# Performance work log

Hardware: AMD Instinct MI355X
Metric: run time of the kernel (lower is better)

The kernel has to match this reference:

```python
import jax, jax.numpy as jnp
import numpy as np

NUM_EXPERTS = 64
TOP_K = 2
AUX_COEF = 0.001
Z_COEF = 0.001


def setup_inputs() -> dict:
    key = jax.random.key(0)
    k1, k2 = jax.random.split(key)
    hidden_states = jax.random.normal(k1, (16384, 4096), dtype=jnp.float32)
    W_gate = jax.random.normal(k2, (NUM_EXPERTS, 4096), dtype=jnp.float32) * 0.02
    return {"hidden_states": hidden_states, "W_gate": W_gate}


def reference(hidden_states, W_gate):
    # Gate GEMM: [N, H] x [E, H]^T -> [N, E]
    router_logits = jnp.einsum('nh,eh->ne', hidden_states, W_gate)
    router_probs = jax.nn.softmax(router_logits, axis=-1)

    # Top-k selection + renormalization
    expert_weights, expert_indices = jax.lax.top_k(router_probs, TOP_K)
    expert_weights = expert_weights / jnp.sum(expert_weights, axis=-1, keepdims=True)

    # Load-balancing loss: num_experts * sum_i f_i * P_i
    num_tokens = router_probs.shape[0]
    one_hot = jax.nn.one_hot(expert_indices, NUM_EXPERTS, dtype=jnp.float32)  # [N, K, E]
    tokens_per_expert = one_hot.sum(axis=(0, 1))  # [E]
    f = tokens_per_expert / (num_tokens * TOP_K)
    P = router_probs.mean(axis=0)
    lb_loss = NUM_EXPERTS * jnp.sum(f * P)

    # Z-loss: mean of logsumexp(logits)^2
    log_z = jax.nn.logsumexp(router_logits, axis=-1)
    z_loss = jnp.mean(log_z ** 2)

    aux_loss = AUX_COEF * lb_loss + Z_COEF * z_loss
    return expert_weights, expert_indices, aux_loss
```

## Files before the change

### kernel.cpp

```cpp
#include <hip/hip_runtime.h>
#include <hip/hip_bf16.h>

#define NTOK 16384
#define HD   4096
#define NE   64
#define TTILE 32
#define NBLK (NTOK / TTILE)
#define NIT  (HD / 32)

#define SAB 40
#define SL  68

#define WS_ACC_FLOATS 192
#define B_ELEMS (NE * HD)

typedef __bf16 bf16x8 __attribute__((ext_vector_type(8)));
typedef __bf16 bf16x4 __attribute__((ext_vector_type(4)));
typedef float  f32x4  __attribute__((ext_vector_type(4)));

__device__ __forceinline__ f32x4 mfma16(bf16x8 a, bf16x8 b, f32x4 c) {
    return __builtin_amdgcn_mfma_f32_16x16x32_bf16(a, b, c, 0, 0, 0);
}

__device__ __forceinline__ void cvt_split(float4 v, bf16x4& hi, bf16x4& lo) {
    float x[4] = {v.x, v.y, v.z, v.w};
    #pragma unroll
    for (int e = 0; e < 4; ++e) {
        __bf16 h = (__bf16)x[e];
        hi[e] = h;
        lo[e] = (__bf16)(x[e] - (float)h);
    }
}

__global__ void zero_ws_kernel(float* ws) {
    int i = threadIdx.x;
    if (i < 129) ws[i] = 0.0f;
}

__global__ __launch_bounds__(256) void prep_kernel(
    const float* __restrict__ Wg, float* __restrict__ ws)
{
    const int tid = threadIdx.x;
    if (blockIdx.x == 0 && tid < 129) ws[tid] = 0.0f;
    __bf16* Bhi = (__bf16*)(ws + WS_ACC_FLOATS);
    __bf16* Blo = Bhi + B_ELEMS;
    const int i = (blockIdx.x * 256 + tid) * 8;
    float4 v0 = *(const float4*)(Wg + i);
    float4 v1 = *(const float4*)(Wg + i + 4);
    bf16x4 h0, l0, h1, l1;
    cvt_split(v0, h0, l0);
    cvt_split(v1, h1, l1);
    *(bf16x4*)(Bhi + i)     = h0;
    *(bf16x4*)(Bhi + i + 4) = h1;
    *(bf16x4*)(Blo + i)     = l0;
    *(bf16x4*)(Blo + i + 4) = l1;
}

__global__ __launch_bounds__(256) void router_pre_kernel(
    const float* __restrict__ hs,
    const __bf16* __restrict__ Bhi,
    const __bf16* __restrict__ Blo,
    float* __restrict__ out,
    float* __restrict__ ws)
{
    __shared__ __bf16 sAhi[2][TTILE * SAB];
    __shared__ __bf16 sAlo[2][TTILE * SAB];
    __shared__ float  sLog[TTILE * SL];
    __shared__ float  sInv[TTILE];
    __shared__ float  sPp[4 * 64];
    __shared__ float  sCnt[64];
    __shared__ float  sZ;

    const int tid = threadIdx.x;
    const int t0  = blockIdx.x * TTILE;

    if (tid < 64) sCnt[tid] = 0.0f;
    if (tid == 0) sZ = 0.0f;

    const int r1 = tid >> 3;
    const int c4 = (tid & 7) * 4;
    const float* gA = hs + (size_t)(t0 + r1) * HD + c4;
    const int oA = r1 * SAB + c4;

    const int lane = tid & 63;
    const int wv   = tid >> 6;
    const int wr   = (wv >> 1) * 16;
    const int wc   = (wv & 1) * 32;
    const int fm   = lane & 15;
    const int fq   = lane >> 4;
    const int fk   = fq * 8;

    const __bf16* gBh = Bhi + (size_t)(wc + fm) * HD + fk;
    const __bf16* gBl = Blo + (size_t)(wc + fm) * HD + fk;

    f32x4 acc[2];
    acc[0] = (f32x4){0.f, 0.f, 0.f, 0.f};
    acc[1] = (f32x4){0.f, 0.f, 0.f, 0.f};

    {
        float4 a0 = *(const float4*)(gA);
        bf16x4 h, l;
        cvt_split(a0, h, l);
        *(bf16x4*)&sAhi[0][oA] = h;
        *(bf16x4*)&sAlo[0][oA] = l;
    }
    bf16x8 cbh[2], cbl[2];
    cbh[0] = *(const bf16x8*)(gBh);
    cbh[1] = *(const bf16x8*)(gBh + 16 * HD);
    cbl[0] = *(const bf16x8*)(gBl);
    cbl[1] = *(const bf16x8*)(gBl + 16 * HD);
    __syncthreads();

    #pragma unroll 2
    for (int it = 0; it < NIT; ++it) {
        const int cur = it & 1;
        const bool more = (it + 1) < NIT;

        float4 na;
        bf16x8 nbh0, nbh1, nbl0, nbl1;
        if (more) {
            const int k0 = (it + 1) * 32;
            na   = *(const float4*)(gA + k0);
            nbh0 = *(const bf16x8*)(gBh + k0);
            nbh1 = *(const bf16x8*)(gBh + 16 * HD + k0);
            nbl0 = *(const bf16x8*)(gBl + k0);
            nbl1 = *(const bf16x8*)(gBl + 16 * HD + k0);
        }

        bf16x8 ahi, alo;
        {
            const int aoff = (wr + fm) * SAB + fk;
            ahi = *(const bf16x8*)&sAhi[cur][aoff];
            alo = *(const bf16x8*)&sAlo[cur][aoff];
        }
        acc[0] = mfma16(ahi, cbh[0], acc[0]);
        acc[0] = mfma16(ahi, cbl[0], acc[0]);
        acc[0] = mfma16(alo, cbh[0], acc[0]);
        acc[0] = mfma16(alo, cbl[0], acc[0]);
        acc[1] = mfma16(ahi, cbh[1], acc[1]);
        acc[1] = mfma16(ahi, cbl[1], acc[1]);
        acc[1] = mfma16(alo, cbh[1], acc[1]);
        acc[1] = mfma16(alo, cbl[1], acc[1]);

        if (more) {
            bf16x4 h, l;
            cvt_split(na, h, l);
            *(bf16x4*)&sAhi[cur ^ 1][oA] = h;
            *(bf16x4*)&sAlo[cur ^ 1][oA] = l;
            cbh[0] = nbh0; cbh[1] = nbh1;
            cbl[0] = nbl0; cbl[1] = nbl1;
        }
        __syncthreads();
    }

    #pragma unroll
    for (int j = 0; j < 2; ++j)
        #pragma unroll
        for (int r = 0; r < 4; ++r) {
            const int tokl = wr + fq * 4 + r;
            const int expl = wc + j * 16 + fm;
            sLog[tokl * SL + expl] = acc[j][r];
        }
    __syncthreads();

    const int g = tid >> 3;
    const int l = tid & 7;
    float* Lrow = &sLog[g * SL + l * 8];
    float lv[8];
    float m = -3.0e38f;
    #pragma unroll
    for (int c = 0; c < 8; ++c) { lv[c] = Lrow[c]; m = fmaxf(m, lv[c]); }
    m = fmaxf(m, __shfl_xor(m, 1, 64));
    m = fmaxf(m, __shfl_xor(m, 2, 64));
    m = fmaxf(m, __shfl_xor(m, 4, 64));

    float v1 = -3.0e38f, v2 = -3.0e38f; int i1 = 0, i2 = 0;
    float ssum = 0.0f;
    #pragma unroll
    for (int c = 0; c < 8; ++c) {
        const float val = lv[c]; const int idx = l * 8 + c;
        const float ev = __expf(val - m);
        Lrow[c] = ev;
        ssum += ev;
        if (val > v1) { v2 = v1; i2 = i1; v1 = val; i1 = idx; }
        else if (val > v2) { v2 = val; i2 = idx; }
    }
    ssum += __shfl_xor(ssum, 1, 64);
    ssum += __shfl_xor(ssum, 2, 64);
    ssum += __shfl_xor(ssum, 4, 64);

    #pragma unroll
    for (int s = 1; s <= 4; s <<= 1) {
        const float ov1 = __shfl_xor(v1, s, 64);
        const int   oi1 = __shfl_xor(i1, s, 64);
        const float ov2 = __shfl_xor(v2, s, 64);
        const int   oi2 = __shfl_xor(i2, s, 64);
        float n1, n2; int ni1, ni2;
        const bool ofirst = (ov1 > v1) || (ov1 == v1 && oi1 < i1);
        if (ofirst) {
            n1 = ov1; ni1 = oi1;
            const bool osec = (ov2 > v1) || (ov2 == v1 && oi2 < i1);
            n2 = osec ? ov2 : v1; ni2 = osec ? oi2 : i1;
        } else {
            n1 = v1; ni1 = i1;
            const bool asec = (v2 > ov1) || (v2 == ov1 && i2 < oi1);
            n2 = asec ? v2 : ov1; ni2 = asec ? i2 : oi1;
        }
        v1 = n1; i1 = ni1; v2 = n2; i2 = ni2;
    }

    if (l == 0) {
        const float e1 = __expf(v1 - m), e2 = __expf(v2 - m);
        const float winv = 1.0f / (e1 + e2);
        const int token = t0 + g;
        out[2 * token]     = e1 * winv;
        out[2 * token + 1] = e2 * winv;
        out[2 * NTOK + 2 * token]     = (float)i1;
        out[2 * NTOK + 2 * token + 1] = (float)i2;
        const float lse = m + __logf(ssum);
        atomicAdd(&sZ, lse * lse);
        atomicAdd(&sCnt[i1], 1.0f);
        atomicAdd(&sCnt[i2], 1.0f);
        sInv[g] = 1.0f / ssum;
    }
    __syncthreads();

    {
        const int e = tid & 63;
        const int q = tid >> 6;
        float part = 0.0f;
        #pragma unroll
        for (int t = 0; t < 8; ++t) {
            const int tok = q * 8 + t;
            part += sLog[tok * SL + e] * sInv[tok];
        }
        sPp[q * 64 + e] = part;
    }
    __syncthreads();
    if (tid < 64) {
        const float ps = sPp[tid] + sPp[64 + tid] + sPp[128 + tid] + sPp[192 + tid];
        atomicAdd(&ws[tid], ps);
        atomicAdd(&ws[64 + tid], sCnt[tid]);
    }
    if (tid == 0) atomicAdd(&ws[128], sZ);
}

__global__ __launch_bounds__(256) void router_fb_kernel(
    const float* __restrict__ hs,
    const float* __restrict__ Wg,
    float* __restrict__ out,
    float* __restrict__ ws)
{
    __shared__ __bf16 sAhi[2][TTILE * SAB];
    __shared__ __bf16 sAlo[2][TTILE * SAB];
    __shared__ __bf16 sBhi[2][NE * SAB];
    __shared__ __bf16 sBlo[2][NE * SAB];
    __shared__ float  sLog[TTILE * SL];
    __shared__ float  sInv[TTILE];
    __shared__ float  sPp[4 * 64];
    __shared__ float  sCnt[64];
    __shared__ float  sZ;

    const int tid = threadIdx.x;
    const int t0  = blockIdx.x * TTILE;

    if (tid < 64) sCnt[tid] = 0.0f;
    if (tid == 0) sZ = 0.0f;

    const int r1 = tid >> 3;
    const int c4 = (tid & 7) * 4;
    const float* gA = hs + (size_t)(t0 + r1) * HD + c4;
    const float* gB = Wg + (size_t)r1 * HD + c4;
    const int oA  = r1 * SAB + c4;
    const int oB1 = r1 * SAB + c4;
    const int oB2 = (r1 + 32) * SAB + c4;

    const int lane = tid & 63;
    const int wv   = tid >> 6;
    const int wr   = (wv >> 1) * 16;
    const int wc   = (wv & 1) * 32;
    const int fm   = lane & 15;
    const int fq   = lane >> 4;
    const int fk   = fq * 8;

    f32x4 acc[2];
    acc[0] = (f32x4){0.f, 0.f, 0.f, 0.f};
    acc[1] = (f32x4){0.f, 0.f, 0.f, 0.f};

    {
        float4 a0 = *(const float4*)(gA);
        float4 b0 = *(const float4*)(gB);
        float4 b1 = *(const float4*)(gB + 32 * HD);
        bf16x4 h, l;
        cvt_split(a0, h, l); *(bf16x4*)&sAhi[0][oA]  = h; *(bf16x4*)&sAlo[0][oA]  = l;
        cvt_split(b0, h, l); *(bf16x4*)&sBhi[0][oB1] = h; *(bf16x4*)&sBlo[0][oB1] = l;
        cvt_split(b1, h, l); *(bf16x4*)&sBhi[0][oB2] = h; *(bf16x4*)&sBlo[0][oB2] = l;
    }
    __syncthreads();

    for (int it = 0; it < NIT; ++it) {
        const int cur = it & 1;
        const bool more = (it + 1) < NIT;
        float4 na0, nb0, nb1;
        if (more) {
            const int k0 = (it + 1) * 32;
            na0 = *(const float4*)(gA + k0);
            nb0 = *(const float4*)(gB + k0);
            nb1 = *(const float4*)(gB + 32 * HD + k0);
        }

        bf16x8 ahi, alo, bhi[2], blo[2];
        {
            const int aoff = (wr + fm) * SAB + fk;
            ahi = *(const bf16x8*)&sAhi[cur][aoff];
            alo = *(const bf16x8*)&sAlo[cur][aoff];
        }
        #pragma unroll
        for (int j = 0; j < 2; ++j) {
            const int boff = (wc + j * 16 + fm) * SAB + fk;
            bhi[j] = *(const bf16x8*)&sBhi[cur][boff];
            blo[j] = *(const bf16x8*)&sBlo[cur][boff];
        }
        #pragma unroll
        for (int j = 0; j < 2; ++j) {
            acc[j] = mfma16(ahi, bhi[j], acc[j]);
            acc[j] = mfma16(ahi, blo[j], acc[j]);
            acc[j] = mfma16(alo, bhi[j], acc[j]);
            acc[j] = mfma16(alo, blo[j], acc[j]);
        }

        if (more) {
            const int nb = cur ^ 1;
            bf16x4 h, l;
            cvt_split(na0, h, l); *(bf16x4*)&sAhi[nb][oA]  = h; *(bf16x4*)&sAlo[nb][oA]  = l;
            cvt_split(nb0, h, l); *(bf16x4*)&sBhi[nb][oB1] = h; *(bf16x4*)&sBlo[nb][oB1] = l;
            cvt_split(nb1, h, l); *(bf16x4*)&sBhi[nb][oB2] = h; *(bf16x4*)&sBlo[nb][oB2] = l;
        }
        __syncthreads();
    }

    #pragma unroll
    for (int j = 0; j < 2; ++j)
        #pragma unroll
        for (int r = 0; r < 4; ++r) {
            const int tokl = wr + fq * 4 + r;
            const int expl = wc + j * 16 + fm;
            sLog[tokl * SL + expl] = acc[j][r];
        }
    __syncthreads();

    const int g = tid >> 3;
    const int l = tid & 7;
    float* Lrow = &sLog[g * SL + l * 8];
    float lv[8];
    float m = -3.0e38f;
    #pragma unroll
    for (int c = 0; c < 8; ++c) { lv[c] = Lrow[c]; m = fmaxf(m, lv[c]); }
    m = fmaxf(m, __shfl_xor(m, 1, 64));
    m = fmaxf(m, __shfl_xor(m, 2, 64));
    m = fmaxf(m, __shfl_xor(m, 4, 64));

    float v1 = -3.0e38f, v2 = -3.0e38f; int i1 = 0, i2 = 0;
    float ssum = 0.0f;
    #pragma unroll
    for (int c = 0; c < 8; ++c) {
        const float val = lv[c]; const int idx = l * 8 + c;
        const float ev = __expf(val - m);
        Lrow[c] = ev;
        ssum += ev;
        if (val > v1) { v2 = v1; i2 = i1; v1 = val; i1 = idx; }
        else if (val > v2) { v2 = val; i2 = idx; }
    }
    ssum += __shfl_xor(ssum, 1, 64);
    ssum += __shfl_xor(ssum, 2, 64);
    ssum += __shfl_xor(ssum, 4, 64);

    #pragma unroll
    for (int s = 1; s <= 4; s <<= 1) {
        const float ov1 = __shfl_xor(v1, s, 64);
        const int   oi1 = __shfl_xor(i1, s, 64);
        const float ov2 = __shfl_xor(v2, s, 64);
        const int   oi2 = __shfl_xor(i2, s, 64);
        float n1, n2; int ni1, ni2;
        const bool ofirst = (ov1 > v1) || (ov1 == v1 && oi1 < i1);
        if (ofirst) {
            n1 = ov1; ni1 = oi1;
            const bool osec = (ov2 > v1) || (ov2 == v1 && oi2 < i1);
            n2 = osec ? ov2 : v1; ni2 = osec ? oi2 : i1;
        } else {
            n1 = v1; ni1 = i1;
            const bool asec = (v2 > ov1) || (v2 == ov1 && i2 < oi1);
            n2 = asec ? v2 : ov1; ni2 = asec ? i2 : oi1;
        }
        v1 = n1; i1 = ni1; v2 = n2; i2 = ni2;
    }

    if (l == 0) {
        const float e1 = __expf(v1 - m), e2 = __expf(v2 - m);
        const float winv = 1.0f / (e1 + e2);
        const int token = t0 + g;
        out[2 * token]     = e1 * winv;
        out[2 * token + 1] = e2 * winv;
        out[2 * NTOK + 2 * token]     = (float)i1;
        out[2 * NTOK + 2 * token + 1] = (float)i2;
        const float lse = m + __logf(ssum);
        atomicAdd(&sZ, lse * lse);
        atomicAdd(&sCnt[i1], 1.0f);
        atomicAdd(&sCnt[i2], 1.0f);
        sInv[g] = 1.0f / ssum;
    }
    __syncthreads();

    {
        const int e = tid & 63;
        const int q = tid >> 6;
        float part = 0.0f;
        #pragma unroll
        for (int t = 0; t < 8; ++t) {
            const int tok = q * 8 + t;
            part += sLog[tok * SL + e] * sInv[tok];
        }
        sPp[q * 64 + e] = part;
    }
    __syncthreads();
    if (tid < 64) {
        const float ps = sPp[tid] + sPp[64 + tid] + sPp[128 + tid] + sPp[192 + tid];
        atomicAdd(&ws[tid], ps);
        atomicAdd(&ws[64 + tid], sCnt[tid]);
    }
    if (tid == 0) atomicAdd(&ws[128], sZ);
}

__global__ void finalize_kernel(const float* __restrict__ ws, float* __restrict__ out) {
    const int e = threadIdx.x;
    const float P = ws[e] * (1.0f / NTOK);
    const float f = ws[64 + e] * (1.0f / (NTOK * 2));
    float term = f * P;
    #pragma unroll
    for (int s = 32; s >= 1; s >>= 1) term += __shfl_xor(term, s, 64);
    if (e == 0) {
        const float lb = 64.0f * term;
        const float z  = ws[128] * (1.0f / NTOK);
        out[4 * NTOK] = 0.001f * lb + 0.001f * z;
    }
}

extern "C" void kernel_launch(void* const* d_in, const int* in_sizes, int n_in,
                              void* d_out, int out_size, void* d_ws, size_t ws_size,
                              hipStream_t stream) {
    const float* hs = (const float*)d_in[0];
    const float* Wg = (const float*)d_in[1];
    float* out = (float*)d_out;
    float* ws  = (float*)d_ws;

    const size_t need = (size_t)WS_ACC_FLOATS * sizeof(float)
                      + (size_t)B_ELEMS * 2 * sizeof(__bf16);
    if (ws_size >= need) {
        const __bf16* Bhi = (const __bf16*)(ws + WS_ACC_FLOATS);
        const __bf16* Blo = Bhi + B_ELEMS;
        hipLaunchKernelGGL(prep_kernel, dim3(128), dim3(256), 0, stream, Wg, ws);
        hipLaunchKernelGGL(router_pre_kernel, dim3(NBLK), dim3(256), 0, stream,
                           hs, Bhi, Blo, out, ws);
    } else {
        hipLaunchKernelGGL(zero_ws_kernel, dim3(1), dim3(256), 0, stream, ws);
        hipLaunchKernelGGL(router_fb_kernel, dim3(NBLK), dim3(256), 0, stream,
                           hs, Wg, out, ws);
    }
    hipLaunchKernelGGL(finalize_kernel, dim3(1), dim3(64), 0, stream, ws, out);
}
```

Baseline: 437.1 us.

## Rewrite pre-split router GEMM as register-pipelined 16-token tiles without LDS staging

The main router kernel now processes 16 tokens per block, with each of four waves owning 16 experts. Each lane loads its A fragment straight from global memory into registers and converts it to hi/lo bf16 in place, so the shared-memory staging and per-iteration __syncthreads are gone. A four-deep register prefetch ring keeps loads in flight, and launch bounds request higher occupancy. The cost is more register pressure, doubled B-fragment traffic per token (fewer tokens share each B load), and twice as many blocks doing atomics into the workspace.

```diff
diff --git a/kernel.cpp b/kernel.cpp
--- a/kernel.cpp
+++ b/kernel.cpp
@@ -4,9 +4,14 @@
 #define NTOK 16384
 #define HD   4096
 #define NE   64
-#define TTILE 32
-#define NBLK (NTOK / TTILE)
-#define NIT  (HD / 32)
+
+#define TPRE     16
+#define NBLK_PRE (NTOK / TPRE)
+#define KSTEPS   (HD / 32)
+
+#define TFB      32
+#define NBLK_FB  (NTOK / TFB)
+#define NIT      (HD / 32)
 
 #define SAB 40
 #define SL  68
@@ -30,6 +35,16 @@
         hi[e] = h;
         lo[e] = (__bf16)(x[e] - (float)h);
     }
+}
+
+__device__ __forceinline__ void cvt8(float4 x0, float4 x1, bf16x8& hi, bf16x8& lo) {
+    bf16x4 h, l;
+    cvt_split(x0, h, l);
+    #pragma unroll
+    for (int e = 0; e < 4; ++e) { hi[e] = h[e]; lo[e] = l[e]; }
+    cvt_split(x1, h, l);
+    #pragma unroll
+    for (int e = 0; e < 4; ++e) { hi[4 + e] = h[e]; lo[4 + e] = l[e]; }
 }
 
 __global__ void zero_ws_kernel(float* ws) {
@@ -56,23 +71,196 @@
     *(bf16x4*)(Blo + i + 4) = l1;
 }
 
-__global__ __launch_bounds__(256) void router_pre_kernel(
+__global__ __launch_bounds__(256, 4) void router_pre_kernel(
     const float* __restrict__ hs,
     const __bf16* __restrict__ Bhi,
     const __bf16* __restrict__ Blo,
     float* __restrict__ out,
     float* __restrict__ ws)
 {
-    __shared__ __bf16 sAhi[2][TTILE * SAB];
-    __shared__ __bf16 sAlo[2][TTILE * SAB];
-    __shared__ float  sLog[TTILE * SL];
-    __shared__ float  sInv[TTILE];
+    __shared__ float sLog[TPRE * SL];
+    __shared__ float sInv[TPRE];
+    __shared__ float sPp[4 * 64];
+    __shared__ float sCnt[64];
+    __shared__ float sZ;
+
+    const int tid = threadIdx.x;
+    const int t0  = blockIdx.x * TPRE;
+
+    if (tid < 64) sCnt[tid] = 0.0f;
+    if (tid == 0) sZ = 0.0f;
+
+    const int lane = tid & 63;
+    const int wv   = tid >> 6;
+    const int fm   = lane & 15;
+    const int fq   = lane >> 4;
+    const int fk   = fq * 8;
+
+    const float*  pA  = hs  + (size_t)(t0 + fm) * HD + fk;
+    const __bf16* pBh = Bhi + (size_t)(wv * 16 + fm) * HD + fk;
+    const __bf16* pBl = Blo + (size_t)(wv * 16 + fm) * HD + fk;
+
+    f32x4 acc = (f32x4){0.f, 0.f, 0.f, 0.f};
+
+    float4 fa0[4], fa1[4];
+    bf16x8 fbh[4], fbl[4];
+
+    #pragma unroll
+    for (int i = 0; i < 4; ++i) {
+        fa0[i] = *(const float4*)(pA + i * 32);
+        fa1[i] = *(const float4*)(pA + i * 32 + 4);
+        fbh[i] = *(const bf16x8*)(pBh + i * 32);
+        fbl[i] = *(const bf16x8*)(pBl + i * 32);
+    }
+
+#define STEP_LOAD(i, kb)                                                 \
+    {                                                                    \
+        bf16x8 ahi, alo;                                                 \
+        cvt8(fa0[i], fa1[i], ahi, alo);                                  \
+        acc = mfma16(ahi, fbh[i], acc);                                  \
+        acc = mfma16(ahi, fbl[i], acc);                                  \
+        acc = mfma16(alo, fbh[i], acc);                                  \
+        acc = mfma16(alo, fbl[i], acc);                                  \
+        const int nks = (kb) + (i) + 4;                                  \
+        fa0[i] = *(const float4*)(pA + nks * 32);                        \
+        fa1[i] = *(const float4*)(pA + nks * 32 + 4);                    \
+        fbh[i] = *(const bf16x8*)(pBh + nks * 32);                       \
+        fbl[i] = *(const bf16x8*)(pBl + nks * 32);                       \
+    }
+#define STEP_NOLOAD(i)                                                   \
+    {                                                                    \
+        bf16x8 ahi, alo;                                                 \
+        cvt8(fa0[i], fa1[i], ahi, alo);                                  \
+        acc = mfma16(ahi, fbh[i], acc);                                  \
+        acc = mfma16(ahi, fbl[i], acc);                                  \
+        acc = mfma16(alo, fbh[i], acc);                                  \
+        acc = mfma16(alo, fbl[i], acc);                                  \
+    }
+
+    for (int it = 0; it < (KSTEPS / 4) - 1; ++it) {
+        const int kb = it * 4;
+        STEP_LOAD(0, kb)
+        STEP_LOAD(1, kb)
+        STEP_LOAD(2, kb)
+        STEP_LOAD(3, kb)
+    }
+    STEP_NOLOAD(0)
+    STEP_NOLOAD(1)
+    STEP_NOLOAD(2)
+    STEP_NOLOAD(3)
+#undef STEP_LOAD
+#undef STEP_NOLOAD
+
+    #pragma unroll
+    for (int r = 0; r < 4; ++r) {
+        const int tokl = fq * 4 + r;
+        const int expl = wv * 16 + fm;
+        sLog[tokl * SL + expl] = acc[r];
+    }
+    __syncthreads();
+
+    const int g = tid >> 4;
+    const int l = tid & 15;
+    float* Lrow = &sLog[g * SL + l * 4];
+    float lv[4];
+    float m = -3.0e38f;
+    #pragma unroll
+    for (int c = 0; c < 4; ++c) { lv[c] = Lrow[c]; m = fmaxf(m, lv[c]); }
+    m = fmaxf(m, __shfl_xor(m, 1, 64));
+    m = fmaxf(m, __shfl_xor(m, 2, 64));
+    m = fmaxf(m, __shfl_xor(m, 4, 64));
+    m = fmaxf(m, __shfl_xor(m, 8, 64));
+
+    float v1 = -3.0e38f, v2 = -3.0e38f; int i1 = 0, i2 = 0;
+    float ssum = 0.0f;
+    #pragma unroll
+    for (int c = 0; c < 4; ++c) {
+        const float val = lv[c]; const int idx = l * 4 + c;
+        const float ev = __expf(val - m);
+        Lrow[c] = ev;
+        ssum += ev;
+        if (val > v1) { v2 = v1; i2 = i1; v1 = val; i1 = idx; }
+        else if (val > v2) { v2 = val; i2 = idx; }
+    }
+    ssum += __shfl_xor(ssum, 1, 64);
+    ssum += __shfl_xor(ssum, 2, 64);
+    ssum += __shfl_xor(ssum, 4, 64);
+    ssum += __shfl_xor(ssum, 8, 64);
+
+    #pragma unroll
+    for (int s = 1; s <= 8; s <<= 1) {
+        const float ov1 = __shfl_xor(v1, s, 64);
+        const int   oi1 = __shfl_xor(i1, s, 64);
+        const float ov2 = __shfl_xor(v2, s, 64);
+        const int   oi2 = __shfl_xor(i2, s, 64);
+        float n1, n2; int ni1, ni2;
+        const bool ofirst = (ov1 > v1) || (ov1 == v1 && oi1 < i1);
+        if (ofirst) {
+            n1 = ov1; ni1 = oi1;
+            const bool osec = (ov2 > v1) || (ov2 == v1 && oi2 < i1);
+            n2 = osec ? ov2 : v1; ni2 = osec ? oi2 : i1;
+        } else {
+            n1 = v1; ni1 = i1;
+            const bool asec = (v2 > ov1) || (v2 == ov1 && i2 < oi1);
+            n2 = asec ? v2 : ov1; ni2 = asec ? i2 : oi1;
+        }
+        v1 = n1; i1 = ni1; v2 = n2; i2 = ni2;
+    }
+
+    if (l == 0) {
+        const float e1 = __expf(v1 - m), e2 = __expf(v2 - m);
+        const float winv = 1.0f / (e1 + e2);
+        const int token = t0 + g;
+        out[2 * token]     = e1 * winv;
+        out[2 * token + 1] = e2 * winv;
+        out[2 * NTOK + 2 * token]     = (float)i1;
+        out[2 * NTOK + 2 * token + 1] = (float)i2;
+        const float lse = m + __logf(ssum);
+        atomicAdd(&sZ, lse * lse);
+        atomicAdd(&sCnt[i1], 1.0f);
+        atomicAdd(&sCnt[i2], 1.0f);
+        sInv[g] = 1.0f / ssum;
+    }
+    __syncthreads();
+
+    {
+        const int e = tid & 63;
+        const int q = tid >> 6;
+        float part = 0.0f;
+        #pragma unroll
+        for (int t = 0; t < 4; ++t) {
+            const int tok = q * 4 + t;
+            part += sLog[tok * SL + e] * sInv[tok];
+        }
+        sPp[q * 64 + e] = part;
+    }
+    __syncthreads();
+    if (tid < 64) {
+        const float ps = sPp[tid] + sPp[64 + tid] + sPp[128 + tid] + sPp[192 + tid];
+        atomicAdd(&ws[tid], ps);
+        atomicAdd(&ws[64 + tid], sCnt[tid]);
+    }
+    if (tid == 0) atomicAdd(&ws[128], sZ);
+}
+
+__global__ __launch_bounds__(256) void router_fb_kernel(
+    const float* __restrict__ hs,
+    const float* __restrict__ Wg,
+    float* __restrict__ out,
+    float* __restrict__ ws)
+{
+    __shared__ __bf16 sAhi[2][TFB * SAB];
+    __shared__ __bf16 sAlo[2][TFB * SAB];
+    __shared__ __bf16 sBhi[2][NE * SAB];
+    __shared__ __bf16 sBlo[2][NE * SAB];
+    __shared__ float  sLog[TFB * SL];
+    __shared__ float  sInv[TFB];
     __shared__ float  sPp[4 * 64];
     __shared__ float  sCnt[64];
     __shared__ float  sZ;
 
     const int tid = threadIdx.x;
-    const int t0  = blockIdx.x * TTILE;
+    const int t0  = blockIdx.x * TFB;
 
     if (tid < 64) sCnt[tid] = 0.0f;
     if (tid == 0) sZ = 0.0f;
@@ -80,7 +268,10 @@
     const int r1 = tid >> 3;
     const int c4 = (tid & 7) * 4;
     const float* gA = hs + (size_t)(t0 + r1) * HD + c4;
-    const int oA = r1 * SAB + c4;
+    const float* gB = Wg + (size_t)r1 * HD + c4;
+    const int oA  = r1 * SAB + c4;
+    const int oB1 = r1 * SAB + c4;
+    const int oB2 = (r1 + 32) * SAB + c4;
 
     const int lane = tid & 63;
     const int wv   = tid >> 6;
@@ -90,65 +281,58 @@
     const int fq   = lane >> 4;
     const int fk   = fq * 8;
 
-    const __bf16* gBh = Bhi + (size_t)(wc + fm) * HD + fk;
-    const __bf16* gBl = Blo + (size_t)(wc + fm) * HD + fk;
-
     f32x4 acc[2];
     acc[0] = (f32x4){0.f, 0.f, 0.f, 0.f};
     acc[1] = (f32x4){0.f, 0.f, 0.f, 0.f};
 
     {
         float4 a0 = *(const float4*)(gA);
+        float4 b0 = *(const float4*)(gB);
+        float4 b1 = *(const float4*)(gB + 32 * HD);
         bf16x4 h, l;
-        cvt_split(a0, h, l);
-        *(bf16x4*)&sAhi[0][oA] = h;
-        *(bf16x4*)&sAlo[0][oA] = l;
-    }
-    bf16x8 cbh[2], cbl[2];
-    cbh[0] = *(const bf16x8*)(gBh);
-    cbh[1] = *(const bf16x8*)(gBh + 16 * HD);
-    cbl[0] = *(const bf16x8*)(gBl);
-    cbl[1] = *(const bf16x8*)(gBl + 16 * HD);
-    __syncthreads();
-
-    #pragma unroll 2
+        cvt_split(a0, h, l); *(bf16x4*)&sAhi[0][oA]  = h; *(bf16x4*)&sAlo[0][oA]  = l;
+        cvt_split(b0, h, l); *(bf16x4*)&sBhi[0][oB1] = h; *(bf16x4*)&sBlo[0][oB1] = l;
+        cvt_split(b1, h, l); *(bf16x4*)&sBhi[0][oB2] = h; *(bf16x4*)&sBlo[0][oB2] = l;
+    }
+    __syncthreads();
+
     for (int it = 0; it < NIT; ++it) {
         const int cur = it & 1;
         const bool more = (it + 1) < NIT;
-
-        float4 na;
-        bf16x8 nbh0, nbh1, nbl0, nbl1;
+        float4 na0, nb0, nb1;
         if (more) {
             const int k0 = (it + 1) * 32;
-            na   = *(const float4*)(gA + k0);
-            nbh0 = *(const bf16x8*)(gBh + k0);
-            nbh1 = *(const bf16x8*)(gBh + 16 * HD + k0);
-            nbl0 = *(const bf16x8*)(gBl + k0);
-            nbl1 = *(const bf16x8*)(gBl + 16 * HD + k0);
-        }
-
-        bf16x8 ahi, alo;
+            na0 = *(const float4*)(gA + k0);
+            nb0 = *(const float4*)(gB + k0);
+            nb1 = *(const float4*)(gB + 32 * HD + k0);
+        }
+
+        bf16x8 ahi, alo, bhi[2], blo[2];
         {
             const int aoff = (wr + fm) * SAB + fk;
             ahi = *(const bf16x8*)&sAhi[cur][aoff];
             alo = *(const bf16x8*)&sAlo[cur][aoff];
         }
-        acc[0] = mfma16(ahi, cbh[0], acc[0]);
-        acc[0] = mfma16(ahi, cbl[0], acc[0]);
-        acc[0] = mfma16(alo, cbh[0], acc[0]);
-        acc[0] = mfma16(alo, cbl[0], acc[0]);
-        acc[1] = mfma16(ahi, cbh[1], acc[1]);
-        acc[1] = mfma16(ahi, cbl[1], acc[1]);
-        acc[1] = mfma16(alo, cbh[1], acc[1]);
-        acc[1] = mfma16(alo, cbl[1], acc[1]);
+        #pragma unroll
+        for (int j = 0; j < 2; ++j) {
+            const int boff = (wc + j * 16 + fm) * SAB + fk;
+            bhi[j] = *(const bf16x8*)&sBhi[cur][boff];
+            blo[j] = *(const bf16x8*)&sBlo[cur][boff];
+        }
+        #pragma unroll
+        for (int j = 0; j < 2; ++j) {
+            acc[j] = mfma16(ahi, bhi[j], acc[j]);
+            acc[j] = mfma16(ahi, blo[j], acc[j]);
+            acc[j] = mfma16(alo, bhi[j], acc[j]);
+            acc[j] = mfma16(alo, blo[j], acc[j]);
+        }
 
         if (more) {
+            const int nb = cur ^ 1;
             bf16x4 h, l;
-            cvt_split(na, h, l);
-            *(bf16x4*)&sAhi[cur ^ 1][oA] = h;
-            *(bf16x4*)&sAlo[cur ^ 1][oA] = l;
-            cbh[0] = nbh0; cbh[1] = nbh1;
-            cbl[0] = nbl0; cbl[1] = nbl1;
+            cvt_split(na0, h, l); *(bf16x4*)&sAhi[nb][oA]  = h; *(bf16x4*)&sAlo[nb][oA]  = l;
+            cvt_split(nb0, h, l); *(bf16x4*)&sBhi[nb][oB1] = h; *(bf16x4*)&sBlo[nb][oB1] = l;
+            cvt_split(nb1, h, l); *(bf16x4*)&sBhi[nb][oB2] = h; *(bf16x4*)&sBlo[nb][oB2] = l;
         }
         __syncthreads();
     }
@@ -245,192 +429,6 @@
     if (tid == 0) atomicAdd(&ws[128], sZ);
 }
 
-__global__ __launch_bounds__(256) void router_fb_kernel(
-    const float* __restrict__ hs,
-    const float* __restrict__ Wg,
-    float* __restrict__ out,
-    float* __restrict__ ws)
-{
-    __shared__ __bf16 sAhi[2][TTILE * SAB];
-    __shared__ __bf16 sAlo[2][TTILE * SAB];
-    __shared__ __bf16 sBhi[2][NE * SAB];
-    __shared__ __bf16 sBlo[2][NE * SAB];
-    __shared__ float  sLog[TTILE * SL];
-    __shared__ float  sInv[TTILE];
-    __shared__ float  sPp[4 * 64];
-    __shared__ float  sCnt[64];
-    __shared__ float  sZ;
-
-    const int tid = threadIdx.x;
-    const int t0  = blockIdx.x * TTILE;
-
-    if (tid < 64) sCnt[tid] = 0.0f;
-    if (tid == 0) sZ = 0.0f;
-
-    const int r1 = tid >> 3;
-    const int c4 = (tid & 7) * 4;
-    const float* gA = hs + (size_t)(t0 + r1) * HD + c4;
-    const float* gB = Wg + (size_t)r1 * HD + c4;
-    const int oA  = r1 * SAB + c4;
-    const int oB1 = r1 * SAB + c4;
-    const int oB2 = (r1 + 32) * SAB + c4;
-
-    const int lane = tid & 63;
-    const int wv   = tid >> 6;
-    const int wr   = (wv >> 1) * 16;
-    const int wc   = (wv & 1) * 32;
-    const int fm   = lane & 15;
-    const int fq   = lane >> 4;
-    const int fk   = fq * 8;
-
-    f32x4 acc[2];
-    acc[0] = (f32x4){0.f, 0.f, 0.f, 0.f};
-    acc[1] = (f32x4){0.f, 0.f, 0.f, 0.f};
-
-    {
-        float4 a0 = *(const float4*)(gA);
-        float4 b0 = *(const float4*)(gB);
-        float4 b1 = *(const float4*)(gB + 32 * HD);
-        bf16x4 h, l;
-        cvt_split(a0, h, l); *(bf16x4*)&sAhi[0][oA]  = h; *(bf16x4*)&sAlo[0][oA]  = l;
-        cvt_split(b0, h, l); *(bf16x4*)&sBhi[0][oB1] = h; *(bf16x4*)&sBlo[0][oB1] = l;
-        cvt_split(b1, h, l); *(bf16x4*)&sBhi[0][oB2] = h; *(bf16x4*)&sBlo[0][oB2] = l;
-    }
-    __syncthreads();
-
-    for (int it = 0; it < NIT; ++it) {
-        const int cur = it & 1;
-        const bool more = (it + 1) < NIT;
-        float4 na0, nb0, nb1;
-        if (more) {
-            const int k0 = (it + 1) * 32;
-            na0 = *(const float4*)(gA + k0);
-            nb0 = *(const float4*)(gB + k0);
-            nb1 = *(const float4*)(gB + 32 * HD + k0);
-        }
-
-        bf16x8 ahi, alo, bhi[2], blo[2];
-        {
-            const int aoff = (wr + fm) * SAB + fk;
-            ahi = *(const bf16x8*)&sAhi[cur][aoff];
-            alo = *(const bf16x8*)&sAlo[cur][aoff];
-        }
-        #pragma unroll
-        for (int j = 0; j < 2; ++j) {
-            const int boff = (wc + j * 16 + fm) * SAB + fk;
-            bhi[j] = *(const bf16x8*)&sBhi[cur][boff];
-            blo[j] = *(const bf16x8*)&sBlo[cur][boff];
-        }
-        #pragma unroll
-        for (int j = 0; j < 2; ++j) {
-            acc[j] = mfma16(ahi, bhi[j], acc[j]);
-            acc[j] = mfma16(ahi, blo[j], acc[j]);
-            acc[j] = mfma16(alo, bhi[j], acc[j]);
-            acc[j] = mfma16(alo, blo[j], acc[j]);
-        }
-
-        if (more) {
-            const int nb = cur ^ 1;
-            bf16x4 h, l;
-            cvt_split(na0, h, l); *(bf16x4*)&sAhi[nb][oA]  = h; *(bf16x4*)&sAlo[nb][oA]  = l;
-            cvt_split(nb0, h, l); *(bf16x4*)&sBhi[nb][oB1] = h; *(bf16x4*)&sBlo[nb][oB1] = l;
-            cvt_split(nb1, h, l); *(bf16x4*)&sBhi[nb][oB2] = h; *(bf16x4*)&sBlo[nb][oB2] = l;
-        }
-        __syncthreads();
-    }
-
-    #pragma unroll
-    for (int j = 0; j < 2; ++j)
-        #pragma unroll
-        for (int r = 0; r < 4; ++r) {
-            const int tokl = wr + fq * 4 + r;
-            const int expl = wc + j * 16 + fm;
-            sLog[tokl * SL + expl] = acc[j][r];
-        }
-    __syncthreads();
-
-    const int g = tid >> 3;
-    const int l = tid & 7;
-    float* Lrow = &sLog[g * SL + l * 8];
-    float lv[8];
-    float m = -3.0e38f;
-    #pragma unroll
-    for (int c = 0; c < 8; ++c) { lv[c] = Lrow[c]; m = fmaxf(m, lv[c]); }
-    m = fmaxf(m, __shfl_xor(m, 1, 64));
-    m = fmaxf(m, __shfl_xor(m, 2, 64));
-    m = fmaxf(m, __shfl_xor(m, 4, 64));
-
-    float v1 = -3.0e38f, v2 = -3.0e38f; int i1 = 0, i2 = 0;
-    float ssum = 0.0f;
-    #pragma unroll
-    for (int c = 0; c < 8; ++c) {
-        const float val = lv[c]; const int idx = l * 8 + c;
-        const float ev = __expf(val - m);
-        Lrow[c] = ev;
-        ssum += ev;
-        if (val > v1) { v2 = v1; i2 = i1; v1 = val; i1 = idx; }
-        else if (val > v2) { v2 = val; i2 = idx; }
-    }
-    ssum += __shfl_xor(ssum, 1, 64);
-    ssum += __shfl_xor(ssum, 2, 64);
-    ssum += __shfl_xor(ssum, 4, 64);
-
-    #pragma unroll
-    for (int s = 1; s <= 4; s <<= 1) {
-        const float ov1 = __shfl_xor(v1, s, 64);
-        const int   oi1 = __shfl_xor(i1, s, 64);
-        const float ov2 = __shfl_xor(v2, s, 64);
-        const int   oi2 = __shfl_xor(i2, s, 64);
-        float n1, n2; int ni1, ni2;
-        const bool ofirst = (ov1 > v1) || (ov1 == v1 && oi1 < i1);
-        if (ofirst) {
-            n1 = ov1; ni1 = oi1;
-            const bool osec = (ov2 > v1) || (ov2 == v1 && oi2 < i1);
-            n2 = osec ? ov2 : v1; ni2 = osec ? oi2 : i1;
-        } else {
-            n1 = v1; ni1 = i1;
-            const bool asec = (v2 > ov1) || (v2 == ov1 && i2 < oi1);
-            n2 = asec ? v2 : ov1; ni2 = asec ? i2 : oi1;
-        }
-        v1 = n1; i1 = ni1; v2 = n2; i2 = ni2;
-    }
-
-    if (l == 0) {
-        const float e1 = __expf(v1 - m), e2 = __expf(v2 - m);
-        const float winv = 1.0f / (e1 + e2);
-        const int token = t0 + g;
-        out[2 * token]     = e1 * winv;
-        out[2 * token + 1] = e2 * winv;
-        out[2 * NTOK + 2 * token]     = (float)i1;
-        out[2 * NTOK + 2 * token + 1] = (float)i2;
-        const float lse = m + __logf(ssum);
-        atomicAdd(&sZ, lse * lse);
-        atomicAdd(&sCnt[i1], 1.0f);
-        atomicAdd(&sCnt[i2], 1.0f);
-        sInv[g] = 1.0f / ssum;
-    }
-    __syncthreads();
-
-    {
-        const int e = tid & 63;
-        const int q = tid >> 6;
-        float part = 0.0f;
-        #pragma unroll
-        for (int t = 0; t < 8; ++t) {
-            const int tok = q * 8 + t;
-            part += sLog[tok * SL + e] * sInv[tok];
-        }
-        sPp[q * 64 + e] = part;
-    }
-    __syncthreads();
-    if (tid < 64) {
-        const float ps = sPp[tid] + sPp[64 + tid] + sPp[128 + tid] + sPp[192 + tid];
-        atomicAdd(&ws[tid], ps);
-        atomicAdd(&ws[64 + tid], sCnt[tid]);
-    }
-    if (tid == 0) atomicAdd(&ws[128], sZ);
-}
-
 __global__ void finalize_kernel(const float* __restrict__ ws, float* __restrict__ out) {
     const int e = threadIdx.x;
     const float P = ws[e] * (1.0f / NTOK);
@@ -459,11 +457,11 @@
         const __bf16* Bhi = (const __bf16*)(ws + WS_ACC_FLOATS);
         const __bf16* Blo = Bhi + B_ELEMS;
         hipLaunchKernelGGL(prep_kernel, dim3(128), dim3(256), 0, stream, Wg, ws);
-        hipLaunchKernelGGL(router_pre_kernel, dim3(NBLK), dim3(256), 0, stream,
+        hipLaunchKernelGGL(router_pre_kernel, dim3(NBLK_PRE), dim3(256), 0, stream,
                            hs, Bhi, Blo, out, ws);
     } else {
         hipLaunchKernelGGL(zero_ws_kernel, dim3(1), dim3(256), 0, stream, ws);
-        hipLaunchKernelGGL(router_fb_kernel, dim3(NBLK), dim3(256), 0, stream,
+        hipLaunchKernelGGL(router_fb_kernel, dim3(NBLK_FB), dim3(256), 0, stream,
                            hs, Wg, out, ws);
     }
     hipLaunchKernelGGL(finalize_kernel, dim3(1), dim3(64), 0, stream, ws, out);
```

Result: slower. 509.5 us (+16.6%).

## Stage W_gate tiles in LDS and double K-step to 64 per iteration

Applied to the files above, without the earlier changes.

The gate weight hi/lo bf16 splits are now loaded cooperatively into double-buffered shared memory instead of each wave fetching its own fragments directly from global memory. The K step per iteration doubles to 64, which halves the number of barriers and loop iterations. A tokens loads 8 floats per thread with wider bf16x8 stores. This adds LDS traffic and shared memory footprint, which may lower occupancy, in exchange for fewer redundant global B reads and less synchronisation.

```diff
diff --git a/kernel.cpp b/kernel.cpp
--- a/kernel.cpp
+++ b/kernel.cpp
@@ -4,11 +4,16 @@
 #define NTOK 16384
 #define HD   4096
 #define NE   64
+
 #define TTILE 32
 #define NBLK (NTOK / TTILE)
+#define BK    64
+#define NITP  (HD / BK)
+
 #define NIT  (HD / 32)
 
 #define SAB 40
+#define SA2 72
 #define SL  68
 
 #define WS_ACC_FLOATS 192
@@ -30,6 +35,16 @@
         hi[e] = h;
         lo[e] = (__bf16)(x[e] - (float)h);
     }
+}
+
+__device__ __forceinline__ void cvt8(float4 x0, float4 x1, bf16x8& hi, bf16x8& lo) {
+    bf16x4 h, l;
+    cvt_split(x0, h, l);
+    #pragma unroll
+    for (int e = 0; e < 4; ++e) { hi[e] = h[e]; lo[e] = l[e]; }
+    cvt_split(x1, h, l);
+    #pragma unroll
+    for (int e = 0; e < 4; ++e) { hi[4 + e] = h[e]; lo[4 + e] = l[e]; }
 }
 
 __global__ void zero_ws_kernel(float* ws) {
@@ -63,8 +78,10 @@
     float* __restrict__ out,
     float* __restrict__ ws)
 {
-    __shared__ __bf16 sAhi[2][TTILE * SAB];
-    __shared__ __bf16 sAlo[2][TTILE * SAB];
+    __shared__ __bf16 sAhi[2][TTILE * SA2];
+    __shared__ __bf16 sAlo[2][TTILE * SA2];
+    __shared__ __bf16 sBhi[2][NE * SA2];
+    __shared__ __bf16 sBlo[2][NE * SA2];
     __shared__ float  sLog[TTILE * SL];
     __shared__ float  sInv[TTILE];
     __shared__ float  sPp[4 * 64];
@@ -77,10 +94,16 @@
     if (tid < 64) sCnt[tid] = 0.0f;
     if (tid == 0) sZ = 0.0f;
 
-    const int r1 = tid >> 3;
-    const int c4 = (tid & 7) * 4;
-    const float* gA = hs + (size_t)(t0 + r1) * HD + c4;
-    const int oA = r1 * SAB + c4;
+    const int rowA = tid >> 3;
+    const int colA = (tid & 7) * 8;
+    const float* gA = hs + (size_t)(t0 + rowA) * HD + colA;
+    const int oAw = rowA * SA2 + colA;
+
+    const int eb = tid >> 2;
+    const int cB = (tid & 3) * 8;
+    const __bf16* gBh = Bhi + (size_t)eb * HD + cB;
+    const __bf16* gBl = Blo + (size_t)eb * HD + cB;
+    const int oBw = eb * SA2 + cB;
 
     const int lane = tid & 63;
     const int wv   = tid >> 6;
@@ -90,65 +113,72 @@
     const int fq   = lane >> 4;
     const int fk   = fq * 8;
 
-    const __bf16* gBh = Bhi + (size_t)(wc + fm) * HD + fk;
-    const __bf16* gBl = Blo + (size_t)(wc + fm) * HD + fk;
-
     f32x4 acc[2];
     acc[0] = (f32x4){0.f, 0.f, 0.f, 0.f};
     acc[1] = (f32x4){0.f, 0.f, 0.f, 0.f};
 
     {
         float4 a0 = *(const float4*)(gA);
-        bf16x4 h, l;
-        cvt_split(a0, h, l);
-        *(bf16x4*)&sAhi[0][oA] = h;
-        *(bf16x4*)&sAlo[0][oA] = l;
-    }
-    bf16x8 cbh[2], cbl[2];
-    cbh[0] = *(const bf16x8*)(gBh);
-    cbh[1] = *(const bf16x8*)(gBh + 16 * HD);
-    cbl[0] = *(const bf16x8*)(gBl);
-    cbl[1] = *(const bf16x8*)(gBl + 16 * HD);
+        float4 a1 = *(const float4*)(gA + 4);
+        bf16x8 h, l;
+        cvt8(a0, a1, h, l);
+        *(bf16x8*)&sAhi[0][oAw] = h;
+        *(bf16x8*)&sAlo[0][oAw] = l;
+        *(bf16x8*)&sBhi[0][oBw]      = *(const bf16x8*)(gBh);
+        *(bf16x8*)&sBhi[0][oBw + 32] = *(const bf16x8*)(gBh + 32);
+        *(bf16x8*)&sBlo[0][oBw]      = *(const bf16x8*)(gBl);
+        *(bf16x8*)&sBlo[0][oBw + 32] = *(const bf16x8*)(gBl + 32);
+    }
     __syncthreads();
 
     #pragma unroll 2
-    for (int it = 0; it < NIT; ++it) {
+    for (int it = 0; it < NITP; ++it) {
         const int cur = it & 1;
-        const bool more = (it + 1) < NIT;
-
-        float4 na;
-        bf16x8 nbh0, nbh1, nbl0, nbl1;
+        const bool more = (it + 1) < NITP;
+
+        float4 na0, na1;
+        bf16x8 nb0, nb1, nb2, nb3;
         if (more) {
-            const int k0 = (it + 1) * 32;
-            na   = *(const float4*)(gA + k0);
-            nbh0 = *(const bf16x8*)(gBh + k0);
-            nbh1 = *(const bf16x8*)(gBh + 16 * HD + k0);
-            nbl0 = *(const bf16x8*)(gBl + k0);
-            nbl1 = *(const bf16x8*)(gBl + 16 * HD + k0);
-        }
-
-        bf16x8 ahi, alo;
-        {
-            const int aoff = (wr + fm) * SAB + fk;
-            ahi = *(const bf16x8*)&sAhi[cur][aoff];
-            alo = *(const bf16x8*)&sAlo[cur][aoff];
-        }
-        acc[0] = mfma16(ahi, cbh[0], acc[0]);
-        acc[0] = mfma16(ahi, cbl[0], acc[0]);
-        acc[0] = mfma16(alo, cbh[0], acc[0]);
-        acc[0] = mfma16(alo, cbl[0], acc[0]);
-        acc[1] = mfma16(ahi, cbh[1], acc[1]);
-        acc[1] = mfma16(ahi, cbl[1], acc[1]);
-        acc[1] = mfma16(alo, cbh[1], acc[1]);
-        acc[1] = mfma16(alo, cbl[1], acc[1]);
+            const int k0 = (it + 1) * BK;
+            na0 = *(const float4*)(gA + k0);
+            na1 = *(const float4*)(gA + k0 + 4);
+            nb0 = *(const bf16x8*)(gBh + k0);
+            nb1 = *(const bf16x8*)(gBh + k0 + 32);
+            nb2 = *(const bf16x8*)(gBl + k0);
+            nb3 = *(const bf16x8*)(gBl + k0 + 32);
+        }
+
+        #pragma unroll
+        for (int kk = 0; kk < 2; ++kk) {
+            const int ao = (wr + fm) * SA2 + kk * 32 + fk;
+            bf16x8 ahi = *(const bf16x8*)&sAhi[cur][ao];
+            bf16x8 alo = *(const bf16x8*)&sAlo[cur][ao];
+            const int bo0 = (wc + fm) * SA2 + kk * 32 + fk;
+            const int bo1 = (wc + 16 + fm) * SA2 + kk * 32 + fk;
+            bf16x8 bh0 = *(const bf16x8*)&sBhi[cur][bo0];
+            bf16x8 bh1 = *(const bf16x8*)&sBhi[cur][bo1];
+            bf16x8 bl0 = *(const bf16x8*)&sBlo[cur][bo0];
+            bf16x8 bl1 = *(const bf16x8*)&sBlo[cur][bo1];
+            acc[0] = mfma16(ahi, bh0, acc[0]);
+            acc[1] = mfma16(ahi, bh1, acc[1]);
+            acc[0] = mfma16(ahi, bl0, acc[0]);
+            acc[1] = mfma16(ahi, bl1, acc[1]);
+            acc[0] = mfma16(alo, bh0, acc[0]);
+            acc[1] = mfma16(alo, bh1, acc[1]);
+            acc[0] = mfma16(alo, bl0, acc[0]);
+            acc[1] = mfma16(alo, bl1, acc[1]);
+        }
 
         if (more) {
-            bf16x4 h, l;
-            cvt_split(na, h, l);
-            *(bf16x4*)&sAhi[cur ^ 1][oA] = h;
-            *(bf16x4*)&sAlo[cur ^ 1][oA] = l;
-            cbh[0] = nbh0; cbh[1] = nbh1;
-            cbl[0] = nbl0; cbl[1] = nbl1;
+            const int nb = cur ^ 1;
+            bf16x8 h, l;
+            cvt8(na0, na1, h, l);
+            *(bf16x8*)&sAhi[nb][oAw] = h;
+            *(bf16x8*)&sAlo[nb][oAw] = l;
+            *(bf16x8*)&sBhi[nb][oBw]      = nb0;
+            *(bf16x8*)&sBhi[nb][oBw + 32] = nb1;
+            *(bf16x8*)&sBlo[nb][oBw]      = nb2;
+            *(bf16x8*)&sBlo[nb][oBw + 32] = nb3;
         }
         __syncthreads();
     }
```

After: 394.1 us. 9.8% less time.
